# Performance work log

Measured on AMD Instinct MI355X. Metric: run time of the kernel, lower is better.

Reference implementation:

```python
import jax, jax.numpy as jnp
import numpy as np

B, T, C = 4, 2048, 1024
H, DQK, DV = 16, 64, 64
W_SCALE = 0.02  # keep logits in a sane range (mimics GPT-style init)


def setup_inputs() -> dict:
    key = jax.random.key(0)
    k1, k2, k3, k4, k5 = jax.random.split(key, 5)
    x = jax.random.normal(k1, (B, T, C), dtype=jnp.float32)
    Wq = jax.random.normal(k2, (C, H * DQK), dtype=jnp.float32) * W_SCALE
    Wk = jax.random.normal(k3, (C, H * DQK), dtype=jnp.float32) * W_SCALE
    Wv = jax.random.normal(k4, (C, H * DV), dtype=jnp.float32) * W_SCALE
    Wp = jax.random.normal(k5, (DV, C), dtype=jnp.float32) * W_SCALE
    return {"x": x, "Wq": Wq, "Wk": Wk, "Wv": Wv, "Wp": Wp, "iter_num": 0}


def reference(x, Wq, Wk, Wv, Wp, iter_num):
    b, t, c = x.shape
    # projections, split into heads: [B, H, T, D]
    q = (x @ Wq).reshape(b, t, H, DQK).transpose(0, 2, 1, 3)
    k = (x @ Wk).reshape(b, t, H, DQK).transpose(0, 2, 1, 3)
    v = (x @ Wv).reshape(b, t, H, DV).transpose(0, 2, 1, 3)
    scale = 1.0 / jnp.sqrt(jnp.asarray(DQK, dtype=x.dtype))
    att = jnp.einsum('bhqd,bhkd->bhqk', q, k) * scale  # [B,H,T,T]
    causal = jnp.tril(jnp.ones((t, t), dtype=bool))
    att = jnp.where(causal[None, None, :, :], att, -jnp.inf)
    att = jax.nn.softmax(att, axis=-1)
    # att @ v then SUM over heads (not concat): [B, T, DV]
    y = jnp.einsum('bhqk,bhkd->bqd', att, v)
    return y @ Wp  # [B, T, C]
```

## Files before the change

### kernel.cpp

```cpp
#include <hip/hip_runtime.h>
#include <hip/hip_bf16.h>

#define DEVI __device__ __forceinline__

typedef __bf16 bf16x8 __attribute__((ext_vector_type(8)));
typedef float f32x4 __attribute__((ext_vector_type(4)));

DEVI unsigned short f2bf(float x) {
    union { __hip_bfloat16 h; unsigned short u; } v;
    v.h = __float2bfloat16(x);
    return v.u;
}

DEVI float exp2_fast(float x) {
#if __has_builtin(__builtin_amdgcn_exp2f)
    return __builtin_amdgcn_exp2f(x);
#else
    return exp2f(x);
#endif
}

DEVI void gload16(const void* gsrc, void* lds) {
    __builtin_amdgcn_global_load_lds(
        (const __attribute__((address_space(1))) void*)gsrc,
        (__attribute__((address_space(3))) void*)lds,
        16, 0, 0);
}

#define BARRIER_MEM() asm volatile("s_barrier" ::: "memory")
#define WAITVM(n) asm volatile("s_waitcnt vmcnt(" #n ")" ::: "memory")
#define LGKM0() asm volatile("s_waitcnt lgkmcnt(0)" ::: "memory")


__global__ __launch_bounds__(256) void convert_f32_bf16_vec(
    const float* __restrict__ in, unsigned short* __restrict__ out, int n4) {
    int i = blockIdx.x * 256 + threadIdx.x;
    if (i >= n4) return;
    float4 v = reinterpret_cast<const float4*>(in)[i];
    ushort4 o;
    o.x = f2bf(v.x); o.y = f2bf(v.y); o.z = f2bf(v.z); o.w = f2bf(v.w);
    reinterpret_cast<ushort4*>(out)[i] = o;
}

__global__ __launch_bounds__(256) void transpose_wqkv(
    const float* __restrict__ wq, const float* __restrict__ wk,
    const float* __restrict__ wv, unsigned short* __restrict__ dst) {
    __shared__ unsigned short tile[32][33];
    const float* src = (blockIdx.z == 0) ? wq : (blockIdx.z == 1) ? wk : wv;
    unsigned short* d = dst + blockIdx.z * 1024 * 1024;
    int c0 = blockIdx.x * 32, r0 = blockIdx.y * 32;
    int tx = threadIdx.x & 31, ty = threadIdx.x >> 5;
    #pragma unroll
    for (int i = ty; i < 32; i += 8)
        tile[tx][i] = f2bf(src[(r0 + i) * 1024 + c0 + tx]);
    __syncthreads();
    #pragma unroll
    for (int i = ty; i < 32; i += 8)
        d[(c0 + i) * 1024 + r0 + tx] = tile[i][tx];
}

__global__ __launch_bounds__(256) void transpose_f32_to_bf16t(
    const float* __restrict__ src, unsigned short* __restrict__ dst,
    int R, int Cc) {
    __shared__ unsigned short tile[32][33];
    int c0 = blockIdx.x * 32, r0 = blockIdx.y * 32;
    int tx = threadIdx.x & 31, ty = threadIdx.x >> 5;
    #pragma unroll
    for (int i = ty; i < 32; i += 8)
        tile[tx][i] = f2bf(src[(r0 + i) * Cc + c0 + tx]);
    __syncthreads();
    #pragma unroll
    for (int i = ty; i < 32; i += 8)
        dst[(c0 + i) * R + r0 + tx] = tile[i][tx];
}

__global__ __launch_bounds__(512, 2) void gemm256(
    const unsigned short* __restrict__ A, const unsigned short* __restrict__ Bt,
    unsigned short* __restrict__ q_out, unsigned short* __restrict__ k_out,
    unsigned short* __restrict__ v_out) {
    __shared__ unsigned short Ab[2][128 * 64];
    __shared__ unsigned short Bb[2][192 * 64];

    const int x = blockIdx.x & 7;
    const int j = blockIdx.x >> 3;
    const int bm = (x * 8 + ((j >> 3) & 7)) << 7;
    const int bn = (((j >> 6) << 3) | (j & 7)) * 192;

    const int tid = threadIdx.x;
    const int w = tid >> 6, l = tid & 63;
    const int wm = w >> 2, wn = w & 3;
    const int lc = l & 15, lg = l >> 4;
    const int lr8 = l >> 3;
    const int colsw = 8 * ((l & 7) ^ lr8);

    const unsigned short* gA = A + (size_t)(bm + lr8) * 1024 + colsw;
    const unsigned short* gB = Bt + (size_t)(bn + lr8) * 1024 + colsw;

    const int p16_0 = (lg ^ (lc & 7)) * 16;
    const int p16_1 = ((4 | lg) ^ (lc & 7)) * 16;

    auto STAGE = [&](int bufn, int tt) {
        #pragma unroll
        for (int jj = 0; jj < 2; ++jj) {
            const int r0 = jj * 64 + w * 8;
            gload16(gA + (size_t)r0 * 1024 + tt * 64,
                    (char*)&Ab[bufn][0] + r0 * 128);
        }
        #pragma unroll
        for (int jj = 0; jj < 3; ++jj) {
            const int r0 = jj * 64 + w * 8;
            gload16(gB + (size_t)r0 * 1024 + tt * 64,
                    (char*)&Bb[bufn][0] + r0 * 128);
        }
    };

    bf16x8 a[4][2], b[3][2];
    f32x4 acc[4][3] = {};
    const int nt = 16;

    STAGE(0, 0);

    #pragma unroll 1
    for (int t = 0; t < nt; ++t) {
        const int buf = t & 1;
        WAITVM(0);
        LGKM0();
        BARRIER_MEM();
        if (t + 1 < nt) STAGE(buf ^ 1, t + 1);

        const char* Arow = (const char*)&Ab[buf][0] + (wm * 64 + lc) * 128;
        const char* Brow = (const char*)&Bb[buf][0] + (wn * 48 + lc) * 128;
        #pragma unroll
        for (int fi = 0; fi < 4; ++fi) {
            a[fi][0] = *(const bf16x8*)(Arow + fi * 16 * 128 + p16_0);
            a[fi][1] = *(const bf16x8*)(Arow + fi * 16 * 128 + p16_1);
        }
        #pragma unroll
        for (int ni = 0; ni < 3; ++ni) {
            b[ni][0] = *(const bf16x8*)(Brow + ni * 16 * 128 + p16_0);
            b[ni][1] = *(const bf16x8*)(Brow + ni * 16 * 128 + p16_1);
        }
        __builtin_amdgcn_s_setprio(1);
        #pragma unroll
        for (int fi = 0; fi < 4; ++fi)
            #pragma unroll
            for (int ni = 0; ni < 3; ++ni) {
                acc[fi][ni] = __builtin_amdgcn_mfma_f32_16x16x32_bf16(
                    a[fi][0], b[ni][0], acc[fi][ni], 0, 0, 0);
                acc[fi][ni] = __builtin_amdgcn_mfma_f32_16x16x32_bf16(
                    a[fi][1], b[ni][1], acc[fi][ni], 0, 0, 0);
            }
        __builtin_amdgcn_s_setprio(0);
    }

    #pragma unroll
    for (int ni = 0; ni < 3; ++ni) {
        const int n = bn + wn * 48 + ni * 16 + lc;
        const int which = n >> 10;
        const int rr = n & 1023;
        if (which == 2) {
            #pragma unroll
            for (int fi = 0; fi < 4; ++fi) {
                const int m = bm + wm * 64 + fi * 16 + lg * 4;
                const int bhh = (m >> 11) * 16 + (rr >> 6);
                const int d = rr & 63;
                const int tt = m & 2047;
                ushort4 o;
                o.x = f2bf(acc[fi][ni][0]); o.y = f2bf(acc[fi][ni][1]);
                o.z = f2bf(acc[fi][ni][2]); o.w = f2bf(acc[fi][ni][3]);
                *reinterpret_cast<ushort4*>(
                    &v_out[((size_t)bhh * 64 + d) * 2048 + tt]) = o;
            }
        } else {
            unsigned short* dst = which ? k_out : q_out;
            #pragma unroll
            for (int fi = 0; fi < 4; ++fi)
                #pragma unroll
                for (int r = 0; r < 4; ++r) {
                    const int m = bm + wm * 64 + fi * 16 + lg * 4 + r;
                    dst[(size_t)m * 1024 + rr] = f2bf(acc[fi][ni][r]);
                }
        }
    }
}

template <int EPI>
__global__ __launch_bounds__(256) void gemm_bt(
    const unsigned short* __restrict__ A, const unsigned short* __restrict__ Bt,
    int Mdim, int Ndim, int Kdim,
    unsigned short* __restrict__ q_out, unsigned short* __restrict__ k_out,
    unsigned short* __restrict__ v_out, float* __restrict__ c_out) {
    __shared__ unsigned short As[128 * 32];
    __shared__ unsigned short Bs[128 * 32];
    const int ntn = Ndim >> 7;
    const int bm = (blockIdx.x / ntn) << 7;
    const int bn = (blockIdx.x % ntn) << 7;
    const int tid = threadIdx.x;
    const int w = tid >> 6, l = tid & 63;
    const int wr = w >> 1, wc = w & 1;
    const int lrow = l >> 2, lcb = (l & 3) * 8;
    const int lc = l & 15, lg = l >> 4;

    f32x4 acc[4][4] = {};

    for (int k0 = 0; k0 < Kdim; k0 += 32) {
        __syncthreads();
        #pragma unroll
        for (int i = 0; i < 2; ++i) {
            int j = w * 2 + i;
            gload16(A + (bm + j * 16 + lrow) * Kdim + k0 + lcb, (char*)As + j * 1024);
            gload16(Bt + (bn + j * 16 + lrow) * Kdim + k0 + lcb, (char*)Bs + j * 1024);
        }
        __syncthreads();
        bf16x8 af[4], bfr[4];
        #pragma unroll
        for (int mi = 0; mi < 4; ++mi)
            af[mi] = *reinterpret_cast<const bf16x8*>(&As[(wr * 64 + mi * 16 + lc) * 32 + lg * 8]);
        #pragma unroll
        for (int ni = 0; ni < 4; ++ni)
            bfr[ni] = *reinterpret_cast<const bf16x8*>(&Bs[(wc * 64 + ni * 16 + lc) * 32 + lg * 8]);
        #pragma unroll
        for (int mi = 0; mi < 4; ++mi)
            #pragma unroll
            for (int ni = 0; ni < 4; ++ni)
                acc[mi][ni] = __builtin_amdgcn_mfma_f32_16x16x32_bf16(
                    af[mi], bfr[ni], acc[mi][ni], 0, 0, 0);
    }

    #pragma unroll
    for (int mi = 0; mi < 4; ++mi) {
        #pragma unroll
        for (int ni = 0; ni < 4; ++ni) {
            #pragma unroll
            for (int r = 0; r < 4; ++r) {
                int m = bm + wr * 64 + mi * 16 + lg * 4 + r;
                int n = bn + wc * 64 + ni * 16 + lc;
                float val = acc[mi][ni][r];
                if (EPI == 0) {
                    int which = n >> 10, rr = n & 1023;
                    unsigned short* dst = (which == 0) ? q_out : (which == 1) ? k_out : v_out;
                    dst[m * 1024 + rr] = f2bf(val);
                } else {
                    c_out[m * Ndim + n] = val;
                }
            }
        }
    }
}

__global__ __launch_bounds__(512, 4) void attn_kernel(
    const unsigned short* __restrict__ qb, const unsigned short* __restrict__ kb,
    const unsigned short* __restrict__ vt, unsigned short* __restrict__ ypart) {
    __shared__ unsigned short Ks[3][64 * 64];
    __shared__ unsigned short Vs[3][64 * 64];
    __shared__ unsigned short plds[8][16 * 72];

    const int i = blockIdx.x;
    const int slot = i >> 3;
    const int bh = (i & 7) + ((slot >> 3) << 3);
    const int pr = slot & 7;
    const int b = bh >> 4, h = bh & 15;
    const int tid = threadIdx.x, w = tid >> 6, l = tid & 63;
    const int lc = l & 15, lg = l >> 4;

    const float SCL = 0.125f * 1.44269504f;

    const int rowc = l >> 3;
    const int colsw = 8 * ((l & 7) ^ rowc);
    const unsigned short* kbh = kb + (b * 2048) * 1024 + h * 64;
    const unsigned short* vbh = vt + bh * 64 * 2048;
    const int swz = (lc & 7) * 8;

    unsigned short* pl = &plds[w][0];

    auto STAGE = [&](int bufn, int kt) {
        const int tk0s = kt << 6;
        const int row = w * 8 + rowc;
        gload16(kbh + (tk0s + row) * 1024 + colsw, (char*)&Ks[bufn][0] + w * 1024);
        gload16(vbh + row * 2048 + tk0s + colsw, (char*)&Vs[bufn][0] + w * 1024);
    };

    auto run_pass = [&](int qblk) {
        const int q0 = qblk << 7;
        const int qrowW = q0 + w * 16;

        bf16x8 qf[2];
        {
            const unsigned short* qp =
                qb + (b * 2048 + qrowW + lc) * 1024 + h * 64;
            qf[0] = *reinterpret_cast<const bf16x8*>(qp + lg * 8);
            qf[1] = *reinterpret_cast<const bf16x8*>(qp + 32 + lg * 8);
        }

        f32x4 accO[4] = {};
        float lsum = 0.f;

        const int nkt = 2 * qblk + 2;
        STAGE(0, 0);
        STAGE(1, 1);
        int cur = 0;

        for (int kt = 0; kt < nkt; ++kt) {
            const int tk0 = kt << 6;
            if (kt + 1 < nkt) { WAITVM(2); } else { WAITVM(0); }
            BARRIER_MEM();
            if (kt + 2 < nkt) {
                const int sb = (cur >= 1) ? cur - 1 : cur + 2;
                STAGE(sb, kt + 2);
            }

            if (tk0 <= qrowW + 15) {
                f32x4 s[4] = {};
                #pragma unroll
                for (int ni = 0; ni < 4; ++ni) {
                    const unsigned short* kr = &Ks[cur][(ni * 16 + lc) * 64];
                    bf16x8 kf0 = *reinterpret_cast<const bf16x8*>(&kr[(lg * 8) ^ swz]);
                    bf16x8 kf1 = *reinterpret_cast<const bf16x8*>(&kr[(32 + lg * 8) ^ swz]);
                    s[ni] = __builtin_amdgcn_mfma_f32_16x16x32_bf16(kf0, qf[0], s[ni], 0, 0, 0);
                    s[ni] = __builtin_amdgcn_mfma_f32_16x16x32_bf16(kf1, qf[1], s[ni], 0, 0, 0);
                }
                const bool needmask = (tk0 + 63 > qrowW);
                const int tq = qrowW + lc;
                #pragma unroll
                for (int ni = 0; ni < 4; ++ni) {
                    float pv[4];
                    #pragma unroll
                    for (int r = 0; r < 4; ++r) {
                        float sv = s[ni][r] * SCL;
                        if (needmask) {
                            int tk = tk0 + ni * 16 + lg * 4 + r;
                            sv = (tk > tq) ? -INFINITY : sv;
                        }
                        pv[r] = exp2_fast(sv);
                        lsum += pv[r];
                    }
                    unsigned int w0, w1;
                    asm("v_cvt_pk_bf16_f32 %0, %1, %2" : "=v"(w0) : "v"(pv[0]), "v"(pv[1]));
                    asm("v_cvt_pk_bf16_f32 %0, %1, %2" : "=v"(w1) : "v"(pv[2]), "v"(pv[3]));
                    uint2 pk2; pk2.x = w0; pk2.y = w1;
                    *reinterpret_cast<uint2*>(&pl[lc * 72 + ni * 16 + lg * 4]) = pk2;
                }
                bf16x8 pf0 = *reinterpret_cast<const bf16x8*>(&pl[lc * 72 + lg * 8]);
                bf16x8 pf1 = *reinterpret_cast<const bf16x8*>(&pl[lc * 72 + 32 + lg * 8]);
                #pragma unroll
                for (int ni = 0; ni < 4; ++ni) {
                    const unsigned short* vr = &Vs[cur][(ni * 16 + lc) * 64];
                    bf16x8 vf0 = *reinterpret_cast<const bf16x8*>(&vr[(lg * 8) ^ swz]);
                    bf16x8 vf1 = *reinterpret_cast<const bf16x8*>(&vr[(32 + lg * 8) ^ swz]);
                    accO[ni] = __builtin_amdgcn_mfma_f32_16x16x32_bf16(vf0, pf0, accO[ni], 0, 0, 0);
                    accO[ni] = __builtin_amdgcn_mfma_f32_16x16x32_bf16(vf1, pf1, accO[ni], 0, 0, 0);
                }
            }
            cur = (cur + 1 == 3) ? 0 : cur + 1;
        }
        BARRIER_MEM();

        float tsum = lsum;
        tsum += __shfl_xor(tsum, 16);
        tsum += __shfl_xor(tsum, 32);
        const float rinv = 1.0f / tsum;
        const int tq = qrowW + lc;
        #pragma unroll
        for (int ni = 0; ni < 4; ++ni) {
            ushort4 o;
            o.x = f2bf(accO[ni][0] * rinv);
            o.y = f2bf(accO[ni][1] * rinv);
            o.z = f2bf(accO[ni][2] * rinv);
            o.w = f2bf(accO[ni][3] * rinv);
            *reinterpret_cast<ushort4*>(
                &ypart[(bh * 2048 + tq) * 64 + ni * 16 + lg * 4]) = o;
        }
    };

    run_pass(15 - pr);
    run_pass(pr);
}

__global__ __launch_bounds__(256) void reduce_heads(
    const unsigned short* __restrict__ ypart, unsigned short* __restrict__ yb) {
    int idx = blockIdx.x * 256 + threadIdx.x;
    int d = idx & 63, m = idx >> 6;
    int b = m >> 11, t = m & 2047;
    const unsigned short* p = ypart + ((b * 16) * 2048 + t) * 64 + d;
    float s = 0.f;
    #pragma unroll
    for (int h = 0; h < 16; ++h) {
        union { unsigned short u; __hip_bfloat16 h; } v;
        v.u = p[h * 2048 * 64];
        s += __bfloat162float(v.h);
    }
    yb[idx] = f2bf(s);
}


extern "C" void kernel_launch(void* const* d_in, const int* in_sizes, int n_in,
                              void* d_out, int out_size, void* d_ws, size_t ws_size,
                              hipStream_t stream) {
    const float* x  = (const float*)d_in[0];
    const float* Wq = (const float*)d_in[1];
    const float* Wk = (const float*)d_in[2];
    const float* Wv = (const float*)d_in[3];
    const float* Wp = (const float*)d_in[4];
    float* out = (float*)d_out;

    if (ws_size < 91357184) return;
    char* ws = (char*)d_ws;
    unsigned short* ypart = (unsigned short*)ws;
    unsigned short* xb   = (unsigned short*)ws;
    unsigned short* wt   = (unsigned short*)(ws + 33554432);
    unsigned short* wpt  = (unsigned short*)(ws + 39845888);
    unsigned short* qbf  = (unsigned short*)(ws + 39976960);
    unsigned short* kbf  = (unsigned short*)(ws + 56754176);
    unsigned short* vtb  = (unsigned short*)(ws + 73531392);
    unsigned short* yb   = (unsigned short*)(ws + 90308608);

    convert_f32_bf16_vec<<<8192, 256, 0, stream>>>(x, xb, 2097152);
    transpose_wqkv<<<dim3(32, 32, 3), 256, 0, stream>>>(Wq, Wk, Wv, wt);
    transpose_f32_to_bf16t<<<dim3(32, 2), 256, 0, stream>>>(Wp, wpt, 64, 1024);

    gemm256<<<1024, 512, 0, stream>>>(xb, wt, qbf, kbf, vtb);

    attn_kernel<<<512, 512, 0, stream>>>(qbf, kbf, vtb, ypart);

    reduce_heads<<<2048, 256, 0, stream>>>(ypart, yb);

    gemm_bt<1><<<(8192 / 128) * (1024 / 128), 256, 0, stream>>>(
        yb, wpt, 8192, 1024, 64, nullptr, nullptr, nullptr, out);
}
```

Baseline: 149.6 us.

## Fuse head-sum reduction into output projection GEMM and merge Wp transpose

The separate reduce_heads kernel is removed. The output GEMM now sums the 16 per-head partial outputs directly into a padded LDS A tile, loads the whole K=64 Wp tile once with an XOR-swizzled layout, and runs a single-stage MFMA loop. The Wp transpose is folded into the Wq/Wk/Wv transpose launch as a fourth z-slice. Together these cut two launches and the intermediate yb round trip. The cost is that every column tile of the same row block repeats the head reduction, so ypart is read several times, relying on cache hits.

Measured after the change: 148.5 us. No clear change (-0.7%).

```diff
diff --git a/kernel.cpp b/kernel.cpp
--- a/kernel.cpp
+++ b/kernel.cpp
@@ -10,6 +10,12 @@
     union { __hip_bfloat16 h; unsigned short u; } v;
     v.h = __float2bfloat16(x);
     return v.u;
+}
+
+DEVI float bf2f(unsigned short u) {
+    union { unsigned short u; __hip_bfloat16 h; } v;
+    v.u = u;
+    return __bfloat162float(v.h);
 }
 
 DEVI float exp2_fast(float x) {
@@ -42,12 +48,16 @@
     reinterpret_cast<ushort4*>(out)[i] = o;
 }
 
-__global__ __launch_bounds__(256) void transpose_wqkv(
+__global__ __launch_bounds__(256) void transpose_wqkvp(
     const float* __restrict__ wq, const float* __restrict__ wk,
-    const float* __restrict__ wv, unsigned short* __restrict__ dst) {
+    const float* __restrict__ wv, const float* __restrict__ wp,
+    unsigned short* __restrict__ dst, unsigned short* __restrict__ wpt) {
     __shared__ unsigned short tile[32][33];
-    const float* src = (blockIdx.z == 0) ? wq : (blockIdx.z == 1) ? wk : wv;
-    unsigned short* d = dst + blockIdx.z * 1024 * 1024;
+    const int z = blockIdx.z;
+    if (z == 3 && blockIdx.y >= 2) return;
+    const float* src = (z == 0) ? wq : (z == 1) ? wk : (z == 2) ? wv : wp;
+    const int R = (z == 3) ? 64 : 1024;
+    unsigned short* d = (z == 3) ? wpt : dst + z * 1024 * 1024;
     int c0 = blockIdx.x * 32, r0 = blockIdx.y * 32;
     int tx = threadIdx.x & 31, ty = threadIdx.x >> 5;
     #pragma unroll
@@ -56,22 +66,7 @@
     __syncthreads();
     #pragma unroll
     for (int i = ty; i < 32; i += 8)
-        d[(c0 + i) * 1024 + r0 + tx] = tile[i][tx];
-}
-
-__global__ __launch_bounds__(256) void transpose_f32_to_bf16t(
-    const float* __restrict__ src, unsigned short* __restrict__ dst,
-    int R, int Cc) {
-    __shared__ unsigned short tile[32][33];
-    int c0 = blockIdx.x * 32, r0 = blockIdx.y * 32;
-    int tx = threadIdx.x & 31, ty = threadIdx.x >> 5;
-    #pragma unroll
-    for (int i = ty; i < 32; i += 8)
-        tile[tx][i] = f2bf(src[(r0 + i) * Cc + c0 + tx]);
-    __syncthreads();
-    #pragma unroll
-    for (int i = ty; i < 32; i += 8)
-        dst[(c0 + i) * R + r0 + tx] = tile[i][tx];
+        d[(c0 + i) * R + r0 + tx] = tile[i][tx];
 }
 
 __global__ __launch_bounds__(512, 2) void gemm256(
@@ -184,41 +179,70 @@
     }
 }
 
-template <int EPI>
-__global__ __launch_bounds__(256) void gemm_bt(
-    const unsigned short* __restrict__ A, const unsigned short* __restrict__ Bt,
-    int Mdim, int Ndim, int Kdim,
-    unsigned short* __restrict__ q_out, unsigned short* __restrict__ k_out,
-    unsigned short* __restrict__ v_out, float* __restrict__ c_out) {
-    __shared__ unsigned short As[128 * 32];
-    __shared__ unsigned short Bs[128 * 32];
-    const int ntn = Ndim >> 7;
-    const int bm = (blockIdx.x / ntn) << 7;
-    const int bn = (blockIdx.x % ntn) << 7;
+__global__ __launch_bounds__(256) void gemm_out_fused(
+    const unsigned short* __restrict__ ypart,
+    const unsigned short* __restrict__ wpt,
+    float* __restrict__ out) {
+    __shared__ unsigned short As[128 * 72];
+    __shared__ unsigned short Bs[128 * 64];
+
+    const int x = blockIdx.x & 7;
+    const int j = blockIdx.x >> 3;
+    const int bm = (x * 8 + (j & 7)) << 7;
+    const int bn = (j >> 3) << 7;
+
     const int tid = threadIdx.x;
     const int w = tid >> 6, l = tid & 63;
     const int wr = w >> 1, wc = w & 1;
-    const int lrow = l >> 2, lcb = (l & 3) * 8;
     const int lc = l & 15, lg = l >> 4;
+    const int lr8 = l >> 3;
+    const int colsw = 8 * ((l & 7) ^ lr8);
+
+    const unsigned short* gB = wpt + (size_t)(bn + lr8) * 64 + colsw;
+    #pragma unroll
+    for (int jj = 0; jj < 4; ++jj) {
+        const int r0 = jj * 32 + w * 8;
+        gload16(gB + (size_t)r0 * 64, (char*)Bs + r0 * 128);
+    }
+
+    const int b = bm >> 11, t0 = bm & 2047;
+    const unsigned short* yb0 = ypart + ((size_t)(b * 16) * 2048 + t0) * 64;
+    #pragma unroll
+    for (int it = 0; it < 8; ++it) {
+        const int idx = it * 256 + tid;
+        const int row = idx >> 4;
+        const int d4 = (idx & 15) * 4;
+        float s0 = 0.f, s1 = 0.f, s2 = 0.f, s3 = 0.f;
+        #pragma unroll
+        for (int h = 0; h < 16; ++h) {
+            ushort4 v = *reinterpret_cast<const ushort4*>(
+                yb0 + ((size_t)h * 2048 + row) * 64 + d4);
+            s0 += bf2f(v.x); s1 += bf2f(v.y);
+            s2 += bf2f(v.z); s3 += bf2f(v.w);
+        }
+        ushort4 o;
+        o.x = f2bf(s0); o.y = f2bf(s1); o.z = f2bf(s2); o.w = f2bf(s3);
+        *reinterpret_cast<ushort4*>(&As[row * 72 + d4]) = o;
+    }
+
+    __syncthreads();
+
+    const int p16_0 = (lg ^ (lc & 7)) * 16;
+    const int p16_1 = ((4 | lg) ^ (lc & 7)) * 16;
 
     f32x4 acc[4][4] = {};
-
-    for (int k0 = 0; k0 < Kdim; k0 += 32) {
-        __syncthreads();
-        #pragma unroll
-        for (int i = 0; i < 2; ++i) {
-            int j = w * 2 + i;
-            gload16(A + (bm + j * 16 + lrow) * Kdim + k0 + lcb, (char*)As + j * 1024);
-            gload16(Bt + (bn + j * 16 + lrow) * Kdim + k0 + lcb, (char*)Bs + j * 1024);
-        }
-        __syncthreads();
+    #pragma unroll
+    for (int half = 0; half < 2; ++half) {
+        const int p16 = half ? p16_1 : p16_0;
         bf16x8 af[4], bfr[4];
         #pragma unroll
         for (int mi = 0; mi < 4; ++mi)
-            af[mi] = *reinterpret_cast<const bf16x8*>(&As[(wr * 64 + mi * 16 + lc) * 32 + lg * 8]);
+            af[mi] = *reinterpret_cast<const bf16x8*>(
+                &As[(wr * 64 + mi * 16 + lc) * 72 + half * 32 + lg * 8]);
         #pragma unroll
         for (int ni = 0; ni < 4; ++ni)
-            bfr[ni] = *reinterpret_cast<const bf16x8*>(&Bs[(wc * 64 + ni * 16 + lc) * 32 + lg * 8]);
+            bfr[ni] = *reinterpret_cast<const bf16x8*>(
+                (const char*)Bs + (wc * 64 + ni * 16 + lc) * 128 + p16);
         #pragma unroll
         for (int mi = 0; mi < 4; ++mi)
             #pragma unroll
@@ -228,24 +252,15 @@
     }
 
     #pragma unroll
-    for (int mi = 0; mi < 4; ++mi) {
-        #pragma unroll
-        for (int ni = 0; ni < 4; ++ni) {
+    for (int mi = 0; mi < 4; ++mi)
+        #pragma unroll
+        for (int ni = 0; ni < 4; ++ni)
             #pragma unroll
             for (int r = 0; r < 4; ++r) {
-                int m = bm + wr * 64 + mi * 16 + lg * 4 + r;
-                int n = bn + wc * 64 + ni * 16 + lc;
-                float val = acc[mi][ni][r];
-                if (EPI == 0) {
-                    int which = n >> 10, rr = n & 1023;
-                    unsigned short* dst = (which == 0) ? q_out : (which == 1) ? k_out : v_out;
-                    dst[m * 1024 + rr] = f2bf(val);
-                } else {
-                    c_out[m * Ndim + n] = val;
-                }
+                const int m = bm + wr * 64 + mi * 16 + lg * 4 + r;
+                const int n = bn + wc * 64 + ni * 16 + lc;
+                out[(size_t)m * 1024 + n] = acc[mi][ni][r];
             }
-        }
-    }
 }
 
 __global__ __launch_bounds__(512, 4) void attn_kernel(
@@ -376,22 +391,6 @@
     run_pass(pr);
 }
 
-__global__ __launch_bounds__(256) void reduce_heads(
-    const unsigned short* __restrict__ ypart, unsigned short* __restrict__ yb) {
-    int idx = blockIdx.x * 256 + threadIdx.x;
-    int d = idx & 63, m = idx >> 6;
-    int b = m >> 11, t = m & 2047;
-    const unsigned short* p = ypart + ((b * 16) * 2048 + t) * 64 + d;
-    float s = 0.f;
-    #pragma unroll
-    for (int h = 0; h < 16; ++h) {
-        union { unsigned short u; __hip_bfloat16 h; } v;
-        v.u = p[h * 2048 * 64];
-        s += __bfloat162float(v.h);
-    }
-    yb[idx] = f2bf(s);
-}
-
 
 extern "C" void kernel_launch(void* const* d_in, const int* in_sizes, int n_in,
                               void* d_out, int out_size, void* d_ws, size_t ws_size,
@@ -412,18 +411,13 @@
     unsigned short* qbf  = (unsigned short*)(ws + 39976960);
     unsigned short* kbf  = (unsigned short*)(ws + 56754176);
     unsigned short* vtb  = (unsigned short*)(ws + 73531392);
-    unsigned short* yb   = (unsigned short*)(ws + 90308608);
 
     convert_f32_bf16_vec<<<8192, 256, 0, stream>>>(x, xb, 2097152);
-    transpose_wqkv<<<dim3(32, 32, 3), 256, 0, stream>>>(Wq, Wk, Wv, wt);
-    transpose_f32_to_bf16t<<<dim3(32, 2), 256, 0, stream>>>(Wp, wpt, 64, 1024);
+    transpose_wqkvp<<<dim3(32, 32, 4), 256, 0, stream>>>(Wq, Wk, Wv, Wp, wt, wpt);
 
     gemm256<<<1024, 512, 0, stream>>>(xb, wt, qbf, kbf, vtb);
 
     attn_kernel<<<512, 512, 0, stream>>>(qbf, kbf, vtb, ypart);
 
-    reduce_heads<<<2048, 256, 0, stream>>>(ypart, yb);
-
-    gemm_bt<1><<<(8192 / 128) * (1024 / 128), 256, 0, stream>>>(
-        yb, wpt, 8192, 1024, 64, nullptr, nullptr, nullptr, out);
-}
+    gemm_out_fused<<<512, 256, 0, stream>>>(ypart, wpt, out);
+}
```
